# Optimization experiments

Measured on AMD Instinct MI355X. Metric: run time of the kernel, lower is better.

The kernel has to match this reference:

```python
import jax, jax.numpy as jnp
import numpy as np

T, N, R = 10, 50000, 50000   # time steps, nodes per graph, total restaurants
D_IN, D, H = 128, 64, 4      # input dim, hidden dim, attention heads
E = 400000                   # edges per timestep (before self-loops)
HD = D // H                  # head dim


def setup_inputs() -> dict:
    key = jax.random.key(0)
    ks = jax.random.split(key, 16)
    inp = {}
    inp["x"] = jax.random.normal(ks[0], (T, N, D_IN), jnp.float32)
    inp["edge_index"] = jax.random.randint(ks[1], (T, 2, E), 0, N, jnp.int32)
    inp["edge_weight"] = jax.random.uniform(ks[2], (T, E), jnp.float32)
    # per-timestep permutation mapping local node idx -> global restaurant idx
    inp["global_idx"] = jax.vmap(lambda k: jax.random.permutation(k, R))(
        jax.random.split(ks[3], T)).astype(jnp.int32)
    s = 0.05
    inp["gcn1_w"] = jax.random.normal(ks[4], (D, D_IN), jnp.float32) * s
    inp["gcn1_b"] = jnp.zeros((D,), jnp.float32)
    inp["gcn2_w"] = jax.random.normal(ks[5], (D, D), jnp.float32) * s
    inp["gcn2_b"] = jnp.zeros((D,), jnp.float32)
    inp["in_proj_w"] = jax.random.normal(ks[6], (3 * D, D), jnp.float32) * s
    inp["in_proj_b"] = jnp.zeros((3 * D,), jnp.float32)
    inp["out_proj_w"] = jax.random.normal(ks[7], (D, D), jnp.float32) * s
    inp["out_proj_b"] = jnp.zeros((D,), jnp.float32)
    inp["w1"] = jnp.ones((T, D), jnp.float32)
    inp["w2"] = jnp.ones((T, D), jnp.float32)
    inp["w3"] = jnp.ones((D,), jnp.float32)
    inp["w4"] = jnp.ones((D,), jnp.float32)
    inp["ln1_g"] = jnp.ones((D,), jnp.float32)
    inp["ln1_b"] = jnp.zeros((D,), jnp.float32)
    inp["ln2_g"] = jnp.ones((D,), jnp.float32)
    inp["ln2_b"] = jnp.zeros((D,), jnp.float32)
    inp["fc_w"] = jax.random.normal(ks[8], (D, D), jnp.float32) * s
    inp["fc_b"] = jnp.zeros((D,), jnp.float32)
    return inp


def _layer_norm(x, g, b, eps=1e-5):
    mu = jnp.mean(x, axis=-1, keepdims=True)
    var = jnp.mean((x - mu) ** 2, axis=-1, keepdims=True)
    return (x - mu) * jax.lax.rsqrt(var + eps) * g + b


def _gcn_layer(h, src, dst, ew, W, b):
    # PyG GCNConv with edge weights; self-loops already appended by caller.
    deg = jax.ops.segment_sum(ew, dst, num_segments=N)
    dinv = jnp.where(deg > 0, jax.lax.rsqrt(deg), 0.0)
    norm = dinv[src] * ew * dinv[dst]                      # [E+N]
    hw = h @ W.T                                           # [N, D]
    agg = jax.ops.segment_sum(norm[:, None] * hw[src], dst, num_segments=N)
    return agg + b


def _forward(x, edge_index, edge_weight, global_idx,
             gcn1_w, gcn1_b, gcn2_w, gcn2_b,
             in_proj_w, in_proj_b, out_proj_w, out_proj_b,
             w1, w2, w3, w4, ln1_g, ln1_b, ln2_g, ln2_b, fc_w, fc_b):
    loop = jnp.arange(N, dtype=edge_index.dtype)
    src = jnp.concatenate([edge_index[:, 0], jnp.broadcast_to(loop, (T, N))], axis=1)
    dst = jnp.concatenate([edge_index[:, 1], jnp.broadcast_to(loop, (T, N))], axis=1)
    ew = jnp.concatenate([edge_weight, jnp.ones((T, N), edge_weight.dtype)], axis=1)

    def per_t(xt, st, dt, wt):
        h = jax.nn.relu(_gcn_layer(xt, st, dt, wt, gcn1_w, gcn1_b))
        return jax.nn.relu(_gcn_layer(h, st, dt, wt, gcn2_w, gcn2_b))

    feat = jax.vmap(per_t)(x, src, dst, ew)                # [T, N, D]

    # scatter local features to global alignment (permutation per timestep)
    aligned = jax.vmap(lambda g, f: jnp.zeros((R, D), f.dtype).at[g].set(f))(
        global_idx, feat)                                  # [T, R, D]
    time_embeds = jnp.transpose(aligned, (1, 0, 2))        # [R, T, D]

    presence = jax.vmap(
        lambda g: jnp.zeros((R,), bool).at[g].set(True))(global_idx)  # [T, R]
    key_padding_mask = ~presence.T                          # [R, T], True = ignore
    bias = jnp.where(key_padding_mask, -1e9, 0.0)           # [R, T]

    # multi-head self-attention over time axis (batch_first, batch = R)
    qkv = time_embeds @ in_proj_w.T + in_proj_b             # [R, T, 3D]
    q, k, v = jnp.split(qkv, 3, axis=-1)
    q = q.reshape(R, T, H, HD)
    k = k.reshape(R, T, H, HD)
    v = v.reshape(R, T, H, HD)
    scores = jnp.einsum('rthd,rshd->rhts', q, k) / np.sqrt(HD)
    scores = scores + bias[:, None, None, :]
    attn = jax.nn.softmax(scores, axis=-1)                  # [R, H, T, T]
    ao = jnp.einsum('rhts,rshd->rthd', attn, v).reshape(R, T, D)
    attn_out = ao @ out_proj_w.T + out_proj_b               # [R, T, D]

    # dropouts are identity in eval mode
    time_feat = _layer_norm(w1 * time_embeds + w2 * attn_out, ln1_g, ln1_b)
    final = time_feat[:, -1, :]                             # [R, D]
    out = final @ fc_w.T + fc_b                             # [R, D]
    return _layer_norm(w3 * final + w4 * out, ln2_g, ln2_b)


def reference(x, edge_index, edge_weight, global_idx,
              gcn1_w, gcn1_b, gcn2_w, gcn2_b,
              in_proj_w, in_proj_b, out_proj_w, out_proj_b,
              w1, w2, w3, w4, ln1_g, ln1_b, ln2_g, ln2_b, fc_w, fc_b):
    return _forward(x, edge_index, edge_weight, global_idx,
                    gcn1_w, gcn1_b, gcn2_w, gcn2_b,
                    in_proj_w, in_proj_b, out_proj_w, out_proj_b,
                    w1, w2, w3, w4, ln1_g, ln1_b, ln2_g, ln2_b, fc_w, fc_b)
```

## Files before the change

kernel.cpp:

```cpp
#include <hip/hip_runtime.h>
#include <cstdint>
#include <cstddef>

namespace {

constexpr int T = 10;
constexpr int N = 50000;
constexpr int R = 50000;
constexpr int DIN = 128;
constexpr int D = 64;
constexpr int E = 400000;

constexpr int BINS = 8192;
constexpr int NR = 7;
constexpr int SEG = 16;
constexpr int ESEG = E / SEG;
constexpr int EV4 = ESEG / 4;

constexpr float WSCALE = 262144.0f;
constexpr float WINV = 1.0f / 262144.0f;

typedef _Float16 h16;
typedef __attribute__((ext_vector_type(8))) _Float16 f16x8;
typedef __attribute__((ext_vector_type(4))) _Float16 f16x4;
typedef __attribute__((ext_vector_type(4))) float f32x4;

__global__ __launch_bounds__(256) void k_hist(const int* __restrict__ ei,
                                              const float* __restrict__ ew,
                                              unsigned* __restrict__ pu) {
  __shared__ unsigned h[BINS];
  int b = blockIdx.x;
  int s = b % SEG;
  int tr = b / SEG;
  int r = tr % NR;
  int t = tr / NR;
  for (int i = threadIdx.x; i < BINS; i += 256) h[i] = 0u;
  __syncthreads();
  int bin0 = r * BINS;
  const int4* dst4 = (const int4*)(ei + (size_t)t * 2 * E + E + s * ESEG);
  const float4* ew4 = (const float4*)(ew + (size_t)t * E + s * ESEG);
  for (int i = threadIdx.x; i < EV4; i += 256) {
    int4 d = dst4[i];
    float4 w = ew4[i];
    unsigned a0 = (unsigned)(d.x - bin0);
    unsigned a1 = (unsigned)(d.y - bin0);
    unsigned a2 = (unsigned)(d.z - bin0);
    unsigned a3 = (unsigned)(d.w - bin0);
    if (a0 < (unsigned)BINS) atomicAdd(&h[a0], 0x1000000u + (unsigned)fmaf(w.x, WSCALE, 0.5f));
    if (a1 < (unsigned)BINS) atomicAdd(&h[a1], 0x1000000u + (unsigned)fmaf(w.y, WSCALE, 0.5f));
    if (a2 < (unsigned)BINS) atomicAdd(&h[a2], 0x1000000u + (unsigned)fmaf(w.z, WSCALE, 0.5f));
    if (a3 < (unsigned)BINS) atomicAdd(&h[a3], 0x1000000u + (unsigned)fmaf(w.w, WSCALE, 0.5f));
  }
  __syncthreads();
  size_t base = (size_t)b * BINS;
  for (int i = threadIdx.x; i < BINS; i += 256) pu[base + i] = h[i];
}

__global__ __launch_bounds__(256) void k_hreduce(const unsigned* __restrict__ pu,
                                                 int* __restrict__ cnt,
                                                 float* __restrict__ dinv) {
  int i = blockIdx.x * 256 + threadIdx.x;
  if (i >= T * N) return;
  int t = i / N, n = i - t * N;
  int r = n / BINS, rel = n - r * BINS;
  unsigned c = 0;
  unsigned wsum = 0;
  #pragma unroll
  for (int s = 0; s < SEG; ++s) {
    unsigned v = pu[((size_t)((t * NR + r) * SEG + s)) * BINS + rel];
    c += v >> 24;
    wsum += v & 0xFFFFFFu;
  }
  cnt[i] = (int)c;
  dinv[i] = rsqrtf(1.0f + (float)wsum * WINV);
}

__global__ __launch_bounds__(256) void k_scan(const int* __restrict__ cnt,
                                              int* __restrict__ rowptr) {
  int t = blockIdx.x;
  int lane = threadIdx.x & 63, wid = threadIdx.x >> 6;
  __shared__ int wsum[4];
  __shared__ int carry_s;
  if (threadIdx.x == 0) carry_s = 0;
  __syncthreads();
  const int4* cp = (const int4*)(cnt + (size_t)t * N);
  int4* rp = (int4*)(rowptr + (size_t)t * N);
  constexpr int NI4 = N / 4;
  for (int base = 0; base < NI4; base += 256) {
    int i = base + threadIdx.x;
    int4 v = make_int4(0, 0, 0, 0);
    if (i < NI4) v = cp[i];
    int tot = v.x + v.y + v.z + v.w;
    int s = tot;
    #pragma unroll
    for (int off = 1; off < 64; off <<= 1) {
      int u = __shfl_up(s, off, 64);
      if (lane >= off) s += u;
    }
    if (lane == 63) wsum[wid] = s;
    int carry = carry_s;
    __syncthreads();
    int wadd = 0;
    #pragma unroll
    for (int w = 0; w < 4; ++w) if (w < wid) wadd += wsum[w];
    if (i < NI4) {
      int excl = carry + wadd + s - tot;
      int4 o;
      o.x = excl;
      o.y = excl + v.x;
      o.z = o.y + v.y;
      o.w = o.z + v.z;
      rp[i] = o;
    }
    __syncthreads();
    if (threadIdx.x == 0) carry_s = carry + wsum[0] + wsum[1] + wsum[2] + wsum[3];
    __syncthreads();
  }
}

__global__ __launch_bounds__(256) void k_segoff(unsigned* __restrict__ pu,
                                                const int* __restrict__ rowptr) {
  int i = blockIdx.x * 256 + threadIdx.x;
  if (i >= T * N) return;
  int t = i / N, n = i - t * N;
  int r = n / BINS, rel = n - r * BINS;
  unsigned run = (unsigned)rowptr[i];
  #pragma unroll
  for (int s = 0; s < SEG; ++s) {
    size_t base = ((size_t)((t * NR + r) * SEG + s)) * BINS + rel;
    unsigned v = pu[base];
    pu[base] = run;
    run += v >> 24;
  }
}

__global__ __launch_bounds__(256) void k_fill2(const int* __restrict__ ei,
                                               const float* __restrict__ ew,
                                               const unsigned* __restrict__ pu,
                                               int2* __restrict__ pk) {
  __shared__ int cur[BINS];
  int b = blockIdx.x;
  int s = b % SEG;
  int tr = b / SEG;
  int r = tr % NR;
  int t = tr / NR;
  size_t pbase = (size_t)b * BINS;
  for (int i = threadIdx.x; i < BINS; i += 256) cur[i] = (int)pu[pbase + i];
  __syncthreads();
  int bin0 = r * BINS;
  const int4* src4 = (const int4*)(ei + (size_t)t * 2 * E + s * ESEG);
  const int4* dst4 = (const int4*)(ei + (size_t)t * 2 * E + E + s * ESEG);
  const float4* ew4 = (const float4*)(ew + (size_t)t * E + s * ESEG);
  int2* pkt = pk + (size_t)t * E;
  for (int i = threadIdx.x; i < EV4; i += 256) {
    int4 d = dst4[i];
    int4 sv = src4[i];
    float4 w = ew4[i];
    unsigned a0 = (unsigned)(d.x - bin0);
    unsigned a1 = (unsigned)(d.y - bin0);
    unsigned a2 = (unsigned)(d.z - bin0);
    unsigned a3 = (unsigned)(d.w - bin0);
    if (a0 < (unsigned)BINS) {
      int pos = atomicAdd(&cur[a0], 1);
      pkt[pos] = make_int2(sv.x, __float_as_int(w.x));
    }
    if (a1 < (unsigned)BINS) {
      int pos = atomicAdd(&cur[a1], 1);
      pkt[pos] = make_int2(sv.y, __float_as_int(w.y));
    }
    if (a2 < (unsigned)BINS) {
      int pos = atomicAdd(&cur[a2], 1);
      pkt[pos] = make_int2(sv.z, __float_as_int(w.z));
    }
    if (a3 < (unsigned)BINS) {
      int pos = atomicAdd(&cur[a3], 1);
      pkt[pos] = make_int2(sv.w, __float_as_int(w.w));
    }
  }
}

__global__ __launch_bounds__(256) void k_prep(const float* __restrict__ g1w,
                                              const float* __restrict__ g2w,
                                              const float* __restrict__ inw,
                                              const float* __restrict__ outw,
                                              const float* __restrict__ fcw,
                                              h16* __restrict__ Wb) {
  int i = blockIdx.x * 256 + threadIdx.x;
  if (i >= 32768) return;
  const float* src;
  int off;
  if (i < 8192)       { src = g1w;  off = 0; }
  else if (i < 12288) { src = g2w;  off = 8192; }
  else if (i < 24576) { src = inw;  off = 12288; }
  else if (i < 28672) { src = outw; off = 24576; }
  else                { src = fcw;  off = 28672; }
  Wb[i] = (h16)src[i - off];
}

template <int K, int NT, bool F16B, int MODE>
__global__ __launch_bounds__(256) void k_mm(const h16* __restrict__ Wb,
                                            const void* __restrict__ Bv,
                                            const float* __restrict__ biasp,
                                            h16* __restrict__ out,
                                            h16* __restrict__ q9,
                                            int Mwaves) {
  int wv = threadIdx.x >> 6, lane = threadIdx.x & 63;
  int wave = blockIdx.x * 4 + wv;
  if (wave >= Mwaves) return;
  int m0 = wave * 16;
  int half = lane & 15, quad = lane >> 4;
  constexpr int KS = K / 32;
  int m = m0 + half;
  float ds = 1.0f;
  if (MODE == 2) ds = biasp[m];
  f16x8 bfrag[KS];
  if (F16B) {
    const h16* Bp = (const h16*)Bv + (size_t)m * K + quad * 8;
    #pragma unroll
    for (int ks = 0; ks < KS; ++ks) bfrag[ks] = *(const f16x8*)(Bp + ks * 32);
  } else {
    const float* Bp = (const float*)Bv + (size_t)m * K + quad * 8;
    #pragma unroll
    for (int ks = 0; ks < KS; ++ks) {
      float4 f0 = *(const float4*)(Bp + ks * 32);
      float4 f1 = *(const float4*)(Bp + ks * 32 + 4);
      f16x8 b;
      b[0] = (h16)f0.x; b[1] = (h16)f0.y; b[2] = (h16)f0.z; b[3] = (h16)f0.w;
      b[4] = (h16)f1.x; b[5] = (h16)f1.y; b[6] = (h16)f1.z; b[7] = (h16)f1.w;
      bfrag[ks] = b;
    }
  }
  #pragma unroll
  for (int jt = 0; jt < NT; ++jt) {
    f32x4 acc = {0.f, 0.f, 0.f, 0.f};
    const h16* Wp = Wb + (size_t)(jt * 16 + half) * K + quad * 8;
    #pragma unroll
    for (int ks = 0; ks < KS; ++ks) {
      f16x8 afrag = *(const f16x8*)(Wp + ks * 32);
      acc = __builtin_amdgcn_mfma_f32_16x16x32_f16(afrag, bfrag[ks], acc, 0, 0, 0);
    }
    int j = jt * 16 + quad * 4;
    if (MODE == 1) {
      float4 b4 = *(const float4*)(biasp + j);
      acc[0] += b4.x; acc[1] += b4.y; acc[2] += b4.z; acc[3] += b4.w;
    }
    if (MODE == 2) {
      acc[0] *= ds; acc[1] *= ds; acc[2] *= ds; acc[3] *= ds;
    }
    f16x4 o;
    o[0] = (h16)acc[0]; o[1] = (h16)acc[1]; o[2] = (h16)acc[2]; o[3] = (h16)acc[3];
    if (MODE != 1) {
      *(f16x4*)(out + (size_t)m * (NT * 16) + j) = o;
    } else {
      if (jt < 4) {
        if (m % 10 == 9) *(f16x4*)(q9 + (size_t)(m / 10) * 64 + j) = o;
      } else {
        *(f16x4*)(out + (size_t)m * 128 + (j - 64)) = o;
      }
    }
  }
}

template <bool SCATTER>
__global__ __launch_bounds__(256) void k_gather(
    const h16* __restrict__ hw, const int2* __restrict__ pk,
    const float* __restrict__ dinv, const int* __restrict__ rowptr,
    const int* __restrict__ cnt, const float* __restrict__ bias,
    const int* __restrict__ gidx, h16* __restrict__ outp) {
  __shared__ float red[4][8][64];
  int wv = threadIdx.x >> 6, lane = threadIdx.x & 63;
  int t = blockIdx.y;
  int n = blockIdx.x * 4 + wv;
  const h16* hwt = hw + (size_t)t * N * D;
  const int2* pkt = pk + (size_t)t * E;
  float dn = dinv[t * N + n];
  int start = rowptr[t * N + n];
  int m = cnt[t * N + n];
  int grp = lane >> 3, sub = lane & 7;
  f32x4 accL = {0.f, 0.f, 0.f, 0.f};
  f32x4 accH = {0.f, 0.f, 0.f, 0.f};
  for (int e = grp; e < m; e += 8) {
    int2 rec = pkt[start + e];
    float w = __int_as_float(rec.y);
    f16x8 h = *(const f16x8*)(hwt + (size_t)rec.x * D + sub * 8);
    #pragma unroll
    for (int j = 0; j < 4; ++j) accL[j] = fmaf(w, (float)h[j], accL[j]);
    #pragma unroll
    for (int j = 0; j < 4; ++j) accH[j] = fmaf(w, (float)h[j + 4], accH[j]);
  }
  float* rw = &red[wv][grp][sub * 8];
  *(f32x4*)(rw) = accL;
  *(f32x4*)(rw + 4) = accH;
  __builtin_amdgcn_wave_barrier();
  const float* rr = &red[wv][0][lane];
  float s = 0.f;
  #pragma unroll
  for (int g = 0; g < 8; ++g) s += rr[g * 64];
  float selfv = (float)hwt[(size_t)n * D + lane];
  float v = fmaxf(fmaf(dn, s + selfv, bias[lane]), 0.f);
  size_t ro;
  if (SCATTER) {
    int rr2 = gidx[(size_t)t * R + n];
    ro = ((size_t)rr2 * T + t) * D + lane;
  } else {
    ro = ((size_t)t * N + n) * D + lane;
  }
  outp[ro] = (h16)v;
}

__global__ __launch_bounds__(256) void k_attn2(const h16* __restrict__ kv,
                                               const h16* __restrict__ q9,
                                               h16* __restrict__ ao) {
  int wv = threadIdx.x >> 6, lane = threadIdx.x & 63;
  int r = blockIdx.x * 4 + wv;
  if (r >= R) return;
  float qv = (float)q9[(size_t)r * 64 + lane];
  const h16* kvr = kv + (size_t)r * T * 128;
  float sc[T], vv[T];
  #pragma unroll
  for (int s = 0; s < T; ++s) {
    float kk = (float)kvr[s * 128 + lane];
    vv[s] = (float)kvr[s * 128 + 64 + lane];
    float p = qv * kk;
    p += __shfl_xor(p, 8, 16);
    p += __shfl_xor(p, 4, 16);
    p += __shfl_xor(p, 2, 16);
    p += __shfl_xor(p, 1, 16);
    sc[s] = p * 0.25f;
  }
  float mx = sc[0];
  #pragma unroll
  for (int s = 1; s < T; ++s) mx = fmaxf(mx, sc[s]);
  float ssum = 0.f;
  #pragma unroll
  for (int s = 0; s < T; ++s) { sc[s] = expf(sc[s] - mx); ssum += sc[s]; }
  float rinv = 1.0f / ssum;
  float aov = 0.f;
  #pragma unroll
  for (int s = 0; s < T; ++s) aov = fmaf(sc[s] * rinv, vv[s], aov);
  ao[(size_t)r * 64 + lane] = (h16)aov;
}

__global__ __launch_bounds__(256) void k_ln1(const h16* __restrict__ te,
                                             const h16* __restrict__ proj,
                                             const float* __restrict__ outB,
                                             const float* __restrict__ w1,
                                             const float* __restrict__ w2,
                                             const float* __restrict__ g1,
                                             const float* __restrict__ b1,
                                             float* __restrict__ finf,
                                             h16* __restrict__ finb) {
  int wv = threadIdx.x >> 6, lane = threadIdx.x & 63;
  int r = blockIdx.x * 4 + wv;
  if (r >= R) return;
  float t9 = (float)te[((size_t)r * T + (T - 1)) * 64 + lane];
  float pr = (float)proj[(size_t)r * 64 + lane] + outB[lane];
  float pre = w1[(T - 1) * 64 + lane] * t9 + w2[(T - 1) * 64 + lane] * pr;
  float s1 = pre;
  #pragma unroll
  for (int off = 32; off >= 1; off >>= 1) s1 += __shfl_xor(s1, off, 64);
  float mu = s1 * (1.0f / 64.0f);
  float dv = pre - mu;
  float s2 = dv * dv;
  #pragma unroll
  for (int off = 32; off >= 1; off >>= 1) s2 += __shfl_xor(s2, off, 64);
  float rstd = 1.0f / sqrtf(s2 * (1.0f / 64.0f) + 1e-5f);
  float fin = dv * rstd * g1[lane] + b1[lane];
  finf[(size_t)r * 64 + lane] = fin;
  finb[(size_t)r * 64 + lane] = (h16)fin;
}

__global__ __launch_bounds__(256) void k_ln2(const float* __restrict__ finf,
                                             const h16* __restrict__ o2,
                                             const float* __restrict__ fcB,
                                             const float* __restrict__ w3,
                                             const float* __restrict__ w4,
                                             const float* __restrict__ g2,
                                             const float* __restrict__ b2,
                                             float* __restrict__ out) {
  int wv = threadIdx.x >> 6, lane = threadIdx.x & 63;
  int r = blockIdx.x * 4 + wv;
  if (r >= R) return;
  float fin = finf[(size_t)r * 64 + lane];
  float oo = (float)o2[(size_t)r * 64 + lane] + fcB[lane];
  float pre = w3[lane] * fin + w4[lane] * oo;
  float s1 = pre;
  #pragma unroll
  for (int off = 32; off >= 1; off >>= 1) s1 += __shfl_xor(s1, off, 64);
  float mu = s1 * (1.0f / 64.0f);
  float dv = pre - mu;
  float s2 = dv * dv;
  #pragma unroll
  for (int off = 32; off >= 1; off >>= 1) s2 += __shfl_xor(s2, off, 64);
  float rstd = 1.0f / sqrtf(s2 * (1.0f / 64.0f) + 1e-5f);
  out[(size_t)r * 64 + lane] = dv * rstd * g2[lane] + b2[lane];
}

}

extern "C" void kernel_launch(void* const* d_in, const int* in_sizes, int n_in,
                              void* d_out, int out_size, void* d_ws, size_t ws_size,
                              hipStream_t stream) {
  const float* x      = (const float*)d_in[0];
  const int*   ei     = (const int*)d_in[1];
  const float* ew     = (const float*)d_in[2];
  const int*   gidx   = (const int*)d_in[3];
  const float* gcn1_w = (const float*)d_in[4];
  const float* gcn1_b = (const float*)d_in[5];
  const float* gcn2_w = (const float*)d_in[6];
  const float* gcn2_b = (const float*)d_in[7];
  const float* in_w   = (const float*)d_in[8];
  const float* in_b   = (const float*)d_in[9];
  const float* out_w  = (const float*)d_in[10];
  const float* out_b  = (const float*)d_in[11];
  const float* w1     = (const float*)d_in[12];
  const float* w2     = (const float*)d_in[13];
  const float* w3     = (const float*)d_in[14];
  const float* w4     = (const float*)d_in[15];
  const float* ln1_g  = (const float*)d_in[16];
  const float* ln1_b  = (const float*)d_in[17];
  const float* ln2_g  = (const float*)d_in[18];
  const float* ln2_b  = (const float*)d_in[19];
  const float* fc_w   = (const float*)d_in[20];
  const float* fc_b   = (const float*)d_in[21];
  float* outp = (float*)d_out;

  char* ws = (char*)d_ws;
  size_t off = 0;
  auto alloc = [&](size_t bytes) {
    void* p = ws + off;
    off += (bytes + 255) & ~(size_t)255;
    return p;
  };
  h16* h1te = (h16*)alloc(sizeof(h16) * (size_t)T * N * D);
  h16* q9b  = (h16*)alloc(sizeof(h16) * (size_t)R * D);
  h16* aob  = (h16*)alloc(sizeof(h16) * (size_t)R * D);
  h16* proj = (h16*)alloc(sizeof(h16) * (size_t)R * D);
  float* finf = (float*)alloc(sizeof(float) * (size_t)R * D);
  h16* finb = (h16*)alloc(sizeof(h16) * (size_t)R * D);
  h16* o2b  = (h16*)alloc(sizeof(h16) * (size_t)R * D);
  h16* Wb   = (h16*)alloc(sizeof(h16) * 32768);
  size_t u_base = off;
  float* dinv   = (float*)alloc(sizeof(float) * T * N);
  int*   cnt    = (int*)alloc(sizeof(int) * T * N);
  int*   rowptr = (int*)alloc(sizeof(int) * T * N);
  int2*  pk     = (int2*)alloc(sizeof(int2) * (size_t)T * E);
  size_t pu_off = off;
  unsigned* pu  = (unsigned*)alloc(sizeof(unsigned) * (size_t)T * NR * SEG * BINS);
  h16* hw = (h16*)(ws + pu_off);
  size_t hw_end = pu_off + sizeof(h16) * (size_t)T * N * D;
  if (hw_end > off) off = hw_end;
  h16* kv = (h16*)(ws + u_base);
  size_t kv_end = u_base + sizeof(h16) * (size_t)T * N * 128;
  if (kv_end > off) off = kv_end;

  const h16* W1b = Wb;
  const h16* W2b = Wb + 8192;
  const h16* WIb = Wb + 12288;
  const h16* WOb = Wb + 24576;
  const h16* WFb = Wb + 28672;

  const int M = T * N;
  const int MW = M / 16;
  const int RW = R / 16;
  const int PREP_BLOCKS = T * NR * SEG;

  k_hist<<<PREP_BLOCKS, 256, 0, stream>>>(ei, ew, pu);
  k_hreduce<<<(T * N + 255) / 256, 256, 0, stream>>>(pu, cnt, dinv);
  k_scan<<<T, 256, 0, stream>>>(cnt, rowptr);
  k_segoff<<<(T * N + 255) / 256, 256, 0, stream>>>(pu, rowptr);
  k_fill2<<<PREP_BLOCKS, 256, 0, stream>>>(ei, ew, pu, pk);
  k_prep<<<128, 256, 0, stream>>>(gcn1_w, gcn2_w, in_w, out_w, fc_w, Wb);

  dim3 gg(N / 4, T);
  k_mm<DIN, 4, false, 2><<<(MW + 3) / 4, 256, 0, stream>>>(W1b, x, dinv, hw, nullptr, MW);
  k_gather<false><<<gg, 256, 0, stream>>>(hw, pk, dinv, rowptr, cnt, gcn1_b, nullptr, h1te);
  k_mm<D, 4, true, 2><<<(MW + 3) / 4, 256, 0, stream>>>(W2b, h1te, dinv, hw, nullptr, MW);
  k_gather<true><<<gg, 256, 0, stream>>>(hw, pk, dinv, rowptr, cnt, gcn2_b, gidx, h1te);

  k_mm<D, 12, true, 1><<<(MW + 3) / 4, 256, 0, stream>>>(WIb, h1te, in_b, kv, q9b, MW);
  k_attn2<<<(R + 3) / 4, 256, 0, stream>>>(kv, q9b, aob);
  k_mm<D, 4, true, 0><<<(RW + 3) / 4, 256, 0, stream>>>(WOb, aob, nullptr, proj, nullptr, RW);
  k_ln1<<<(R + 3) / 4, 256, 0, stream>>>(h1te, proj, out_b, w1, w2, ln1_g, ln1_b, finf, finb);
  k_mm<D, 4, true, 0><<<(RW + 3) / 4, 256, 0, stream>>>(WFb, finb, nullptr, o2b, nullptr, RW);
  k_ln2<<<(R + 3) / 4, 256, 0, stream>>>(finf, o2b, fc_b, w3, w4, ln2_g, ln2_b, outp);
}
```

Before: 1.194 ms.

## Process two nodes per wave in GCN gather and enlarge histogram bins

```diff
diff --git a/kernel.cpp b/kernel.cpp
--- a/kernel.cpp
+++ b/kernel.cpp
@@ -11,8 +11,8 @@
 constexpr int D = 64;
 constexpr int E = 400000;
 
-constexpr int BINS = 8192;
-constexpr int NR = 7;
+constexpr int BINS = 16384;
+constexpr int NR = 4;
 constexpr int SEG = 16;
 constexpr int ESEG = E / SEG;
 constexpr int EV4 = ESEG / 4;
@@ -267,45 +267,76 @@
     const float* __restrict__ dinv, const int* __restrict__ rowptr,
     const int* __restrict__ cnt, const float* __restrict__ bias,
     const int* __restrict__ gidx, h16* __restrict__ outp) {
-  __shared__ float red[4][8][64];
+  __shared__ __align__(16) float red[4][8][68];
   int wv = threadIdx.x >> 6, lane = threadIdx.x & 63;
   int t = blockIdx.y;
-  int n = blockIdx.x * 4 + wv;
+  int nd = lane >> 5;
+  int grp = (lane >> 3) & 3;
+  int sub = lane & 7;
+  int n = blockIdx.x * 8 + wv * 2 + nd;
   const h16* hwt = hw + (size_t)t * N * D;
   const int2* pkt = pk + (size_t)t * E;
-  float dn = dinv[t * N + n];
   int start = rowptr[t * N + n];
   int m = cnt[t * N + n];
-  int grp = lane >> 3, sub = lane & 7;
+  int nA = blockIdx.x * 8 + wv * 2;
+  int nB = nA + 1;
+  float selfA = (float)hwt[(size_t)nA * D + lane];
+  float selfB = (float)hwt[(size_t)nB * D + lane];
+  float dnA = dinv[t * N + nA];
+  float dnB = dinv[t * N + nB];
+  float bi = bias[lane];
   f32x4 accL = {0.f, 0.f, 0.f, 0.f};
   f32x4 accH = {0.f, 0.f, 0.f, 0.f};
-  for (int e = grp; e < m; e += 8) {
-    int2 rec = pkt[start + e];
-    float w = __int_as_float(rec.y);
-    f16x8 h = *(const f16x8*)(hwt + (size_t)rec.x * D + sub * 8);
-    #pragma unroll
-    for (int j = 0; j < 4; ++j) accL[j] = fmaf(w, (float)h[j], accL[j]);
-    #pragma unroll
-    for (int j = 0; j < 4; ++j) accH[j] = fmaf(w, (float)h[j + 4], accH[j]);
-  }
-  float* rw = &red[wv][grp][sub * 8];
+  int e = grp;
+  for (; e + 4 < m; e += 8) {
+    int2 ra = pkt[start + e];
+    int2 rb = pkt[start + e + 4];
+    float wa = __int_as_float(ra.y);
+    float wb = __int_as_float(rb.y);
+    f16x8 ha = *(const f16x8*)(hwt + (size_t)ra.x * D + sub * 8);
+    f16x8 hb = *(const f16x8*)(hwt + (size_t)rb.x * D + sub * 8);
+    #pragma unroll
+    for (int j = 0; j < 4; ++j) {
+      accL[j] = fmaf(wa, (float)ha[j], accL[j]);
+      accH[j] = fmaf(wa, (float)ha[j + 4], accH[j]);
+    }
+    #pragma unroll
+    for (int j = 0; j < 4; ++j) {
+      accL[j] = fmaf(wb, (float)hb[j], accL[j]);
+      accH[j] = fmaf(wb, (float)hb[j + 4], accH[j]);
+    }
+  }
+  if (e < m) {
+    int2 ra = pkt[start + e];
+    float wa = __int_as_float(ra.y);
+    f16x8 ha = *(const f16x8*)(hwt + (size_t)ra.x * D + sub * 8);
+    #pragma unroll
+    for (int j = 0; j < 4; ++j) {
+      accL[j] = fmaf(wa, (float)ha[j], accL[j]);
+      accH[j] = fmaf(wa, (float)ha[j + 4], accH[j]);
+    }
+  }
+  float* rw = &red[wv][nd * 4 + grp][sub * 8];
   *(f32x4*)(rw) = accL;
   *(f32x4*)(rw + 4) = accH;
   __builtin_amdgcn_wave_barrier();
-  const float* rr = &red[wv][0][lane];
-  float s = 0.f;
-  #pragma unroll
-  for (int g = 0; g < 8; ++g) s += rr[g * 64];
-  float selfv = (float)hwt[(size_t)n * D + lane];
-  float v = fmaxf(fmaf(dn, s + selfv, bias[lane]), 0.f);
-  size_t ro;
-  if (SCATTER) {
-    int rr2 = gidx[(size_t)t * R + n];
-    ro = ((size_t)rr2 * T + t) * D + lane;
-  } else {
-    ro = ((size_t)t * N + n) * D + lane;
-  }
-  outp[ro] = (h16)v;
+  #pragma unroll
+  for (int d2 = 0; d2 < 2; ++d2) {
+    int nn = nA + d2;
+    float s = red[wv][d2 * 4 + 0][lane] + red[wv][d2 * 4 + 1][lane] +
+              red[wv][d2 * 4 + 2][lane] + red[wv][d2 * 4 + 3][lane];
+    float selfv = d2 ? selfB : selfA;
+    float dn = d2 ? dnB : dnA;
+    float v = fmaxf(fmaf(dn, s + selfv, bi), 0.f);
+    size_t ro;
+    if (SCATTER) {
+      int rr2 = gidx[(size_t)t * R + nn];
+      ro = ((size_t)rr2 * T + t) * D + lane;
+    } else {
+      ro = ((size_t)t * N + nn) * D + lane;
+    }
+    outp[ro] = (h16)v;
+  }
 }
 
 __global__ __launch_bounds__(256) void k_attn2(const h16* __restrict__ kv,
@@ -472,7 +503,7 @@
   k_fill2<<<PREP_BLOCKS, 256, 0, stream>>>(ei, ew, pu, pk);
   k_prep<<<128, 256, 0, stream>>>(gcn1_w, gcn2_w, in_w, out_w, fc_w, Wb);
 
-  dim3 gg(N / 4, T);
+  dim3 gg(N / 8, T);
   k_mm<DIN, 4, false, 2><<<(MW + 3) / 4, 256, 0, stream>>>(W1b, x, dinv, hw, nullptr, MW);
   k_gather<false><<<gg, 256, 0, stream>>>(hw, pk, dinv, rowptr, cnt, gcn1_b, nullptr, h1te);
   k_mm<D, 4, true, 2><<<(MW + 3) / 4, 256, 0, stream>>>(W2b, h1te, dinv, hw, nullptr, MW);
```

Result: faster. 1.077 ms (-9.8%).
